# Performance work log

Measured on AMD Instinct MI355X. Metric: run time of the kernel, lower is better.

Reference implementation:

```python
import jax, jax.numpy as jnp
import numpy as np

J = 50
HEADS = 4
DIMS = [3, 64, 128, 256]
POSE_DIM = 512
B, T = 16, 128


def build_edge_index():
    # 49-bone chain over 50 joints, symmetrized, plus self-loops
    # (PyG GATConv adds self-loops by default).
    e = []
    for i in range(J - 1):
        e.append((i, i + 1))
        e.append((i + 1, i))
    for i in range(J):
        e.append((i, i))
    e = sorted(e)
    return jnp.array(e, dtype=jnp.int32).T  # [2, E]


def setup_inputs() -> dict:
    key = jax.random.key(0)
    ks = iter(jax.random.split(key, 64))
    def nrm(shape, s):
        return jax.random.normal(next(ks), shape, jnp.float32) * s
    inp = {"pose_seq": jax.random.normal(next(ks), (B, T, J, 3), jnp.float32)}
    for i in range(3):
        din, dout = DIMS[i], DIMS[i + 1]
        C = dout // HEADS
        inp[f"W{i}"] = nrm((din, dout), din ** -0.5)        # GATConv lin (no bias)
        inp[f"as{i}"] = nrm((HEADS, C), 0.1)                 # att_src
        inp[f"ad{i}"] = nrm((HEADS, C), 0.1)                 # att_dst
        inp[f"bg{i}"] = jnp.zeros((dout,), jnp.float32)      # GATConv bias
        inp[f"R{i}"] = nrm((din, dout), din ** -0.5)         # residual Linear (no bias)
        inp[f"g{i}"] = jnp.ones((dout,), jnp.float32)        # LayerNorm gamma
        inp[f"b{i}"] = jnp.zeros((dout,), jnp.float32)       # LayerNorm beta
    inp["fpW"] = nrm((J * DIMS[-1], POSE_DIM), (J * DIMS[-1]) ** -0.5)
    inp["fpb"] = jnp.zeros((POSE_DIM,), jnp.float32)
    inp["fng"] = jnp.ones((POSE_DIM,), jnp.float32)
    inp["fnb"] = jnp.zeros((POSE_DIM,), jnp.float32)
    inp["edge_index"] = build_edge_index()
    return inp


def _layer_norm(x, g, b, eps=1e-5):
    mu = jnp.mean(x, axis=-1, keepdims=True)
    var = jnp.mean(jnp.square(x - mu), axis=-1, keepdims=True)
    return (x - mu) * jax.lax.rsqrt(var + eps) * g + b


def _gat(x, src, dst, W, a_s, a_d, bias):
    # x: [G, J, Fin]; edges identical across the G graphs.
    G, Jn, _ = x.shape
    H, C = a_s.shape
    h = (x @ W).reshape(G, Jn, H, C)
    es = jnp.einsum('gjhc,hc->gjh', h, a_s)[:, src]   # [G,E,H]
    ed = jnp.einsum('gjhc,hc->gjh', h, a_d)[:, dst]
    e = jax.nn.leaky_relu(es + ed, 0.2)
    # per-destination softmax over incoming edges (per head)
    m = jnp.full((G, Jn, H), -jnp.inf, e.dtype).at[:, dst].max(e)
    m = jax.lax.stop_gradient(m)
    w = jnp.exp(e - m[:, dst])
    den = jnp.zeros((G, Jn, H), e.dtype).at[:, dst].add(w)
    alpha = w / den[:, dst]                            # [G,E,H]
    out = jnp.zeros((G, Jn, H, C), e.dtype).at[:, dst].add(alpha[..., None] * h[:, src])
    return out.reshape(G, Jn, H * C) + bias


def _forward(pose_seq, layers, fpW, fpb, fng, fnb, edge_index):
    Bb, Tt = pose_seq.shape[0], pose_seq.shape[1]
    x = pose_seq.reshape(Bb * Tt, J, 3)
    src, dst = edge_index[0], edge_index[1]
    for (W, a_s, a_d, bg, R, g, b) in layers:
        h = _gat(x, src, dst, W, a_s, a_d, bg)
        res = x @ R  # dims always change -> Linear residual (bias=False)
        x = jax.nn.gelu(_layer_norm(h + res, g, b), approximate=False)
    x = x.reshape(Bb * Tt, J * DIMS[-1]) @ fpW + fpb
    x = _layer_norm(x, fng, fnb)
    return x.reshape(Bb, Tt, POSE_DIM)


def reference(pose_seq, W0, as0, ad0, bg0, R0, g0, b0,
              W1, as1, ad1, bg1, R1, g1, b1,
              W2, as2, ad2, bg2, R2, g2, b2,
              fpW, fpb, fng, fnb, edge_index):
    layers = [(W0, as0, ad0, bg0, R0, g0, b0),
              (W1, as1, ad1, bg1, R1, g1, b1),
              (W2, as2, ad2, bg2, R2, g2, b2)]
    return _forward(pose_seq, layers, fpW, fpb, fng, fnb, edge_index)
```

## Files before the change

kernel.cpp:

```cpp
#include <hip/hip_runtime.h>
#include <hip/hip_bf16.h>
#include <math.h>

#define J 50
#define GN 2048
#define GK 12800
#define GON 512

#define SPLITK 8
#define BKC (GK / SPLITK)
#define NKT (BKC / 64)

typedef short short8 __attribute__((ext_vector_type(8)));
typedef float f32x4 __attribute__((ext_vector_type(4)));

__device__ __forceinline__ float lrelu(float x) { return x > 0.f ? x : 0.2f * x; }
__device__ __forceinline__ ushort f2bu(float f) { __hip_bfloat16 h = __float2bfloat16(f); return *(ushort*)&h; }

__device__ __forceinline__ float gelu_fast(float y) {
    float u = y * (1.f + 0.044715f * y * y);
    float t = __expf(-1.5957691216f * u);
    return y / (1.f + t);
}


template<int DIN, int KPAD, int DOUT, bool LAST>
__device__ __forceinline__ void gat_layer_v3(
    int tid, ushort* xbf, float* esW, float* Acoef, float* statsC, float* statsN,
    const ushort* __restrict__ Wt, const ushort* __restrict__ Rt,
    const ushort* __restrict__ Wex,
    const float* __restrict__ bg, const float* __restrict__ gam,
    const float* __restrict__ bet, ushort* __restrict__ gout)
{
    constexpr int NFW = DOUT / 64;
    constexpr int GRX = KPAD / 8;
    constexpr int XM  = (GRX < 8 ? GRX : 8) - 1;
    constexpr int NKS = KPAD / 32;
    const int lane = tid & 63, w = tid >> 6;
    const int lr = lane & 15, lg = lane >> 4;

    f32x4 acc[4][NFW];
    f32x4 ext[4];

    #pragma unroll
    for (int m = 0; m < 4; ++m) {
        ext[m] = (f32x4){0.f, 0.f, 0.f, 0.f};
        #pragma unroll
        for (int nf = 0; nf < NFW; ++nf) acc[m][nf] = (f32x4){0.f, 0.f, 0.f, 0.f};
    }
    #pragma unroll
    for (int ks = 0; ks < NKS; ++ks) {
        short8 af[4];
        #pragma unroll
        for (int m = 0; m < 4; ++m) {
            int row = m * 16 + lr;
            int g = (ks * 4 + lg) ^ (row & XM);
            af[m] = *(const short8*)&xbf[(row * GRX + g) * 8];
        }
        #pragma unroll
        for (int nf = 0; nf < NFW; ++nf) {
            int col = (w * NFW + nf) * 16 + lr;
            short8 bf = *(const short8*)&Wt[col * KPAD + ks * 32 + lg * 8];
            #pragma unroll
            for (int m = 0; m < 4; ++m)
                acc[m][nf] = __builtin_amdgcn_mfma_f32_16x16x32_bf16(af[m], bf, acc[m][nf], 0, 0, 0);
        }
        short8 bfe = *(const short8*)&Wex[(w * 16 + lr) * KPAD + ks * 32 + lg * 8];
        #pragma unroll
        for (int m = 0; m < 4; ++m)
            ext[m] = __builtin_amdgcn_mfma_f32_16x16x32_bf16(af[m], bfe, ext[m], 0, 0, 0);
    }

    if (lr < 2) {
        float* dstp = &esW[w * 130 + lr * 65];
        #pragma unroll
        for (int m = 0; m < 4; ++m)
            #pragma unroll
            for (int q = 0; q < 4; ++q)
                dstp[m * 16 + lg * 4 + q] = ext[m][q];
    }
    asm volatile("s_waitcnt lgkmcnt(0)" ::: "memory");

    {
        int r = lane;
        const float* ew = &esW[w * 130];
        float es0 = ew[r];
        float esm = ew[r > 0 ? r - 1 : 0];
        float esp = ew[r < 63 ? r + 1 : 63];
        float edj = ew[65 + r];
        float e1 = lrelu(es0 + edj);
        float e0 = (r > 0)     ? lrelu(esm + edj) : -1e30f;
        float e2 = (r < J - 1) ? lrelu(esp + edj) : -1e30f;
        float mx = fmaxf(e1, fmaxf(e0, e2));
        float w0 = __expf(e0 - mx), w1 = __expf(e1 - mx), w2 = __expf(e2 - mx);
        float rden = 1.f / (w0 + w1 + w2);
        Acoef[w * 192 + r]       = w0 * rden;
        Acoef[w * 192 + 64 + r]  = w1 * rden;
        Acoef[w * 192 + 128 + r] = w2 * rden;
    }
    asm volatile("s_waitcnt lgkmcnt(0)" ::: "memory");

    #pragma unroll
    for (int nf = 0; nf < NFW; ++nf) {
        float tmp[4][4];
        #pragma unroll
        for (int m = 0; m < 4; ++m) {
            int rb = m * 16 + lg * 4;
            float4 c0 = *(const float4*)&Acoef[w * 192 + rb];
            float4 c1 = *(const float4*)&Acoef[w * 192 + 64 + rb];
            float4 c2 = *(const float4*)&Acoef[w * 192 + 128 + rb];
            int mp = m > 0 ? m - 1 : 0, mn = m < 3 ? m + 1 : 3;
            float t1 = __shfl(acc[m][nf][3],  (lane + 48) & 63);
            float t2 = __shfl(acc[mp][nf][3], (lane + 48) & 63);
            float hprev = (lg > 0) ? t1 : t2;
            float b1 = __shfl(acc[m][nf][0],  (lane + 16) & 63);
            float b2 = __shfl(acc[mn][nf][0], (lane + 16) & 63);
            float hnext = (lg < 3) ? b1 : b2;
            tmp[m][0] = c0.x * hprev         + c1.x * acc[m][nf][0] + c2.x * acc[m][nf][1];
            tmp[m][1] = c0.y * acc[m][nf][0] + c1.y * acc[m][nf][1] + c2.y * acc[m][nf][2];
            tmp[m][2] = c0.z * acc[m][nf][1] + c1.z * acc[m][nf][2] + c2.z * acc[m][nf][3];
            tmp[m][3] = c0.w * acc[m][nf][2] + c1.w * acc[m][nf][3] + c2.w * hnext;
        }
        #pragma unroll
        for (int m = 0; m < 4; ++m)
            #pragma unroll
            for (int q = 0; q < 4; ++q) acc[m][nf][q] = tmp[m][q];
    }

    #pragma unroll
    for (int ks = 0; ks < NKS; ++ks) {
        short8 af[4];
        #pragma unroll
        for (int m = 0; m < 4; ++m) {
            int row = m * 16 + lr;
            int g = (ks * 4 + lg) ^ (row & XM);
            af[m] = *(const short8*)&xbf[(row * GRX + g) * 8];
        }
        #pragma unroll
        for (int nf = 0; nf < NFW; ++nf) {
            int col = (w * NFW + nf) * 16 + lr;
            short8 bf = *(const short8*)&Rt[col * KPAD + ks * 32 + lg * 8];
            #pragma unroll
            for (int m = 0; m < 4; ++m)
                acc[m][nf] = __builtin_amdgcn_mfma_f32_16x16x32_bf16(af[m], bf, acc[m][nf], 0, 0, 0);
        }
    }
    #pragma unroll
    for (int nf = 0; nf < NFW; ++nf) {
        float bgv = bg[(w * NFW + nf) * 16 + lr];
        #pragma unroll
        for (int m = 0; m < 4; ++m)
            #pragma unroll
            for (int q = 0; q < 4; ++q) acc[m][nf][q] += bgv;
    }

    #pragma unroll
    for (int m = 0; m < 4; ++m)
        #pragma unroll
        for (int q = 0; q < 4; ++q) {
            float s = 0.f, s2 = 0.f;
            #pragma unroll
            for (int nf = 0; nf < NFW; ++nf) {
                float v = acc[m][nf][q];
                s += v; s2 += v * v;
            }
            #pragma unroll
            for (int off = 1; off <= 8; off <<= 1) {
                s  += __shfl_xor(s, off, 64);
                s2 += __shfl_xor(s2, off, 64);
            }
            if (lr == 0) {
                int row = m * 16 + lg * 4 + q;
                atomicAdd(&statsC[row * 2], s);
                atomicAdd(&statsC[row * 2 + 1], s2);
            }
        }
    __syncthreads();
    if (tid < 64) {
        float S = statsC[tid * 2], S2 = statsC[tid * 2 + 1];
        float mu = S * (1.f / DOUT);
        float var = S2 * (1.f / DOUT) - mu * mu;
        statsC[tid * 2] = mu;
        statsC[tid * 2 + 1] = rsqrtf(var + 1e-5f);
    }
    __syncthreads();

    constexpr int NGR = DOUT / 8;
    constexpr int NXM = (NGR < 8 ? NGR : 8) - 1;
    #pragma unroll
    for (int nf = 0; nf < NFW; ++nf) {
        int col = (w * NFW + nf) * 16 + lr;
        float ga = gam[col], be = bet[col];
        #pragma unroll
        for (int m = 0; m < 4; ++m)
            #pragma unroll
            for (int q = 0; q < 4; ++q) {
                int row = m * 16 + lg * 4 + q;
                float mu = statsC[row * 2], inv = statsC[row * 2 + 1];
                float y = (acc[m][nf][q] - mu) * inv * ga + be;
                float ge = gelu_fast(y);
                if (LAST) {
                    if (row < J) gout[row * 256 + col] = f2bu(ge);
                } else {
                    xbf[(row * NGR + ((col >> 3) ^ (row & NXM))) * 8 + (col & 7)] =
                        (row < J) ? f2bu(ge) : (ushort)0;
                }
            }
    }
    if (tid < 128) statsN[tid] = 0.f;
    __syncthreads();
}

__global__ __launch_bounds__(256, 4) void gat_mfma(
    const float* __restrict__ pose,
    const ushort* __restrict__ Wt0, const ushort* __restrict__ Rt0,
    const ushort* __restrict__ Wt1, const ushort* __restrict__ Rt1,
    const ushort* __restrict__ Wt2, const ushort* __restrict__ Rt2,
    const ushort* __restrict__ wex0, const ushort* __restrict__ wex1,
    const ushort* __restrict__ wex2,
    const float* bg0, const float* g0v, const float* b0v,
    const float* bg1, const float* g1v, const float* b1v,
    const float* bg2, const float* g2v, const float* b2v,
    ushort* __restrict__ xg)
{
    __shared__ ushort xbf[64 * 128];
    __shared__ float esW[4 * 130];
    __shared__ float Acoef[4 * 192];
    __shared__ float sA[128], sB[128];
    int g = blockIdx.x, tid = threadIdx.x;

    for (int i = tid; i < 64 * 32; i += 256) {
        int row = i >> 5, c = i & 31;
        float v = (row < J && c < 3) ? pose[(size_t)g * (J * 3) + row * 3 + c] : 0.f;
        xbf[(row * 4 + ((c >> 3) ^ (row & 3))) * 8 + (c & 7)] = f2bu(v);
    }
    if (tid < 128) sA[tid] = 0.f;
    __syncthreads();
    gat_layer_v3<3,   32,  64, false>(tid, xbf, esW, Acoef, sA, sB, Wt0, Rt0, wex0,
                                      bg0, g0v, b0v, nullptr);
    gat_layer_v3<64,  64, 128, false>(tid, xbf, esW, Acoef, sB, sA, Wt1, Rt1, wex1,
                                      bg1, g1v, b1v, nullptr);
    gat_layer_v3<128,128, 256, true >(tid, xbf, esW, Acoef, sA, sB, Wt2, Rt2, wex2,
                                      bg2, g2v, b2v, xg + (size_t)g * GK);
}

__global__ __launch_bounds__(256) void prep_weights(
    const float* __restrict__ W0, const float* __restrict__ R0,
    const float* __restrict__ W1, const float* __restrict__ R1,
    const float* __restrict__ W2, const float* __restrict__ R2,
    ushort* __restrict__ wt)
{
    int i = blockIdx.x * 256 + threadIdx.x;
    if (i < 2048)       { int n = i >> 5, k = i & 31;                    wt[i] = f2bu(k < 3 ? W0[k * 64 + n] : 0.f); }
    else if (i < 4096)  { int j = i - 2048;  int n = j >> 5, k = j & 31; wt[i] = f2bu(k < 3 ? R0[k * 64 + n] : 0.f); }
    else if (i < 12288) { int j = i - 4096;  int n = j >> 6, k = j & 63; wt[i] = f2bu(W1[k * 128 + n]); }
    else if (i < 20480) { int j = i - 12288; int n = j >> 6, k = j & 63; wt[i] = f2bu(R1[k * 128 + n]); }
    else if (i < 53248) { int j = i - 20480; int n = j >> 7, k = j & 127; wt[i] = f2bu(W2[k * 256 + n]); }
    else if (i < 86016) { int j = i - 53248; int n = j >> 7, k = j & 127; wt[i] = f2bu(R2[k * 256 + n]); }
}

__global__ __launch_bounds__(256) void prep_wex(
    const float* __restrict__ as0, const float* __restrict__ ad0, const float* __restrict__ W0,
    const float* __restrict__ as1, const float* __restrict__ ad1, const float* __restrict__ W1,
    const float* __restrict__ as2, const float* __restrict__ ad2, const float* __restrict__ W2,
    ushort* __restrict__ wex0, ushort* __restrict__ wex1, ushort* __restrict__ wex2)
{
    int i = blockIdx.x * 256 + threadIdx.x;
    const float *as_, *ad_, *W; ushort* dst; int KPAD, DIN, DOUT, idx;
    if (i < 2048)       { idx = i;         KPAD = 32;  DIN = 3;   DOUT = 64;  as_ = as0; ad_ = ad0; W = W0; dst = wex0; }
    else if (i < 6144)  { idx = i - 2048;  KPAD = 64;  DIN = 64;  DOUT = 128; as_ = as1; ad_ = ad1; W = W1; dst = wex1; }
    else if (i < 14336) { idx = i - 6144;  KPAD = 128; DIN = 128; DOUT = 256; as_ = as2; ad_ = ad2; W = W2; dst = wex2; }
    else return;
    int k = idx % KPAD;
    int col = (idx / KPAD) & 15;
    int h = idx / (KPAD * 16);
    int C = DOUT / 4;
    float v = 0.f;
    if (col < 2 && k < DIN) {
        const float* a = (col == 0) ? as_ : ad_;
        for (int c = 0; c < C; ++c) v += W[k * DOUT + h * C + c] * a[h * C + c];
    }
    dst[idx] = f2bu(v);
}

__global__ __launch_bounds__(256) void fpw_to_bt(
    const float* __restrict__ fpW, ushort* __restrict__ Bt)
{
    __shared__ float tile[64][65];
    int kb = (blockIdx.x >> 3) * 64;
    int nb = (blockIdx.x & 7) * 64;
    int tid = threadIdx.x;
    #pragma unroll
    for (int i = 0; i < 16; ++i) {
        int idx = tid + i * 256;
        int r = idx >> 6, c = idx & 63;
        tile[r][c] = fpW[(size_t)(kb + r) * GON + nb + c];
    }
    __syncthreads();
    #pragma unroll
    for (int i = 0; i < 16; ++i) {
        int idx = tid + i * 256;
        int nr = idx >> 6, kc = idx & 63;
        Bt[(size_t)(nb + nr) * GK + kb + kc] = f2bu(tile[kc][nr]);
    }
}

__global__ __launch_bounds__(512) void final_gemm_mfma(
    const ushort* __restrict__ A,
    const ushort* __restrict__ Bt,
    float* __restrict__ parts)
{
    __shared__ ushort Asm[2][128 * 64];
    __shared__ ushort Bsm[2][128 * 64];
    int tid = threadIdx.x;
    int bid = blockIdx.x;
    int tileid = bid & 63, sp = bid >> 6;
    int rt = tileid >> 2, ct = tileid & 3;
    int ar0 = rt * 128, bc0 = ct * 128;
    int kbase = sp * BKC;

    int lane = tid & 63, wid = tid >> 6;
    int wm = wid >> 2, wn = wid & 3;

    f32x4 acc[4][2];
    #pragma unroll
    for (int mi = 0; mi < 4; ++mi)
        #pragma unroll
        for (int ni = 0; ni < 2; ++ni)
            acc[mi][ni] = (f32x4){0.f, 0.f, 0.f, 0.f};

#define STAGE(pg, k0)                                                              \
    do {                                                                           \
        _Pragma("unroll")                                                          \
        for (int s_ = 0; s_ < 4; ++s_) {                                           \
            int g_ = tid + s_ * 512;                                               \
            int gg_ = g_ & 1023;                                                   \
            int row_ = gg_ >> 3, cg_ = gg_ & 7;                                    \
            int csw_ = cg_ ^ (row_ & 7);                                           \
            const ushort* src_;                                                    \
            ushort* dst_;                                                          \
            if (g_ < 1024) {                                                       \
                src_ = A + (size_t)(ar0 + row_) * GK + (k0) + csw_ * 8;            \
                dst_ = &Asm[pg][gg_ * 8];                                          \
            } else {                                                               \
                src_ = Bt + (size_t)(bc0 + row_) * GK + (k0) + csw_ * 8;           \
                dst_ = &Bsm[pg][gg_ * 8];                                          \
            }                                                                      \
            __builtin_amdgcn_global_load_lds(                                      \
                (const __attribute__((address_space(1))) void*)src_,               \
                (__attribute__((address_space(3))) void*)dst_, 16, 0, 0);          \
        }                                                                          \
    } while (0)

    STAGE(0, kbase);
    __syncthreads();
    int pg = 0;
    for (int kt = 0; kt < NKT; ++kt) {
        if (kt + 1 < NKT) STAGE(pg ^ 1, kbase + (kt + 1) * 64);
        const ushort* Ab = Asm[pg];
        const ushort* Bb = Bsm[pg];
        short8 afr[4][2], bfr[2][2];
        #pragma unroll
        for (int mi = 0; mi < 4; ++mi)
            #pragma unroll
            for (int ks = 0; ks < 2; ++ks) {
                int row = wm * 64 + mi * 16 + (lane & 15);
                int gs = (ks * 4 + (lane >> 4)) ^ (row & 7);
                afr[mi][ks] = *(const short8*)&Ab[row * 64 + gs * 8];
            }
        #pragma unroll
        for (int ni = 0; ni < 2; ++ni)
            #pragma unroll
            for (int ks = 0; ks < 2; ++ks) {
                int row = wn * 32 + ni * 16 + (lane & 15);
                int gs = (ks * 4 + (lane >> 4)) ^ (row & 7);
                bfr[ni][ks] = *(const short8*)&Bb[row * 64 + gs * 8];
            }
        #pragma unroll
        for (int ks = 0; ks < 2; ++ks)
            #pragma unroll
            for (int mi = 0; mi < 4; ++mi)
                #pragma unroll
                for (int ni = 0; ni < 2; ++ni)
                    acc[mi][ni] = __builtin_amdgcn_mfma_f32_16x16x32_bf16(
                        afr[mi][ks], bfr[ni][ks], acc[mi][ni], 0, 0, 0);
        __syncthreads();
        pg ^= 1;
    }
#undef STAGE

    float* outp = parts + (size_t)sp * GN * GON;
    #pragma unroll
    for (int mi = 0; mi < 4; ++mi)
        #pragma unroll
        for (int ni = 0; ni < 2; ++ni)
            #pragma unroll
            for (int r = 0; r < 4; ++r) {
                int row = ar0 + wm * 64 + mi * 16 + (lane >> 4) * 4 + r;
                int col = bc0 + wn * 32 + ni * 16 + (lane & 15);
                outp[(size_t)row * GON + col] = acc[mi][ni][r];
            }
}

__global__ __launch_bounds__(256) void final_reduce_ln(
    const float* __restrict__ parts, float* __restrict__ out,
    const float* __restrict__ fpb, const float* __restrict__ fng,
    const float* __restrict__ fnb)
{
    int row = blockIdx.x * 4 + (threadIdx.x >> 6);
    int lane = threadIdx.x & 63;
    float v[8];
    float sum = 0.f;
    #pragma unroll
    for (int cc = 0; cc < 8; ++cc) {
        int o = lane + (cc << 6);
        float a = 0.f;
        #pragma unroll
        for (int s = 0; s < SPLITK; ++s)
            a += parts[(size_t)s * GN * GON + (size_t)row * GON + o];
        v[cc] = a + fpb[o];
        sum += v[cc];
    }
    #pragma unroll
    for (int off = 32; off >= 1; off >>= 1) sum += __shfl_xor(sum, off, 64);
    float mu = sum * (1.f / GON);
    float sq = 0.f;
    #pragma unroll
    for (int cc = 0; cc < 8; ++cc) { float d = v[cc] - mu; sq += d * d; }
    #pragma unroll
    for (int off = 32; off >= 1; off >>= 1) sq += __shfl_xor(sq, off, 64);
    float inv = rsqrtf(sq * (1.f / GON) + 1e-5f);
    #pragma unroll
    for (int cc = 0; cc < 8; ++cc) {
        int o = lane + (cc << 6);
        out[(size_t)row * GON + o] = (v[cc] - mu) * inv * fng[o] + fnb[o];
    }
}

extern "C" void kernel_launch(void* const* d_in, const int* in_sizes, int n_in,
                              void* d_out, int out_size, void* d_ws, size_t ws_size,
                              hipStream_t stream) {
    (void)in_sizes; (void)n_in; (void)out_size; (void)ws_size;
    const float* pose = (const float*)d_in[0];
    const float *W0 = (const float*)d_in[1],  *as0 = (const float*)d_in[2],
                *ad0 = (const float*)d_in[3], *bg0 = (const float*)d_in[4],
                *R0 = (const float*)d_in[5],  *g0v = (const float*)d_in[6],
                *b0v = (const float*)d_in[7];
    const float *W1 = (const float*)d_in[8],  *as1 = (const float*)d_in[9],
                *ad1 = (const float*)d_in[10],*bg1 = (const float*)d_in[11],
                *R1 = (const float*)d_in[12], *g1v = (const float*)d_in[13],
                *b1v = (const float*)d_in[14];
    const float *W2 = (const float*)d_in[15], *as2 = (const float*)d_in[16],
                *ad2 = (const float*)d_in[17],*bg2 = (const float*)d_in[18],
                *R2 = (const float*)d_in[19], *g2v = (const float*)d_in[20],
                *b2v = (const float*)d_in[21];
    const float* fpW = (const float*)d_in[22];
    const float* fpb = (const float*)d_in[23];
    const float* fng = (const float*)d_in[24];
    const float* fnb = (const float*)d_in[25];

    ushort* xg = (ushort*)d_ws;
    ushort* Bt = xg + (size_t)GN * GK;
    float* parts = (float*)(Bt + (size_t)GON * GK);
    ushort* wsm = (ushort*)(parts + (size_t)SPLITK * GN * GON);
    ushort *Wt0 = wsm,          *Rt0 = wsm + 2048;
    ushort *Wt1 = wsm + 4096,   *Rt1 = wsm + 12288;
    ushort *Wt2 = wsm + 20480,  *Rt2 = wsm + 53248;
    ushort* wex = wsm + 86016;
    ushort *wex0 = wex, *wex1 = wex + 2048, *wex2 = wex + 6144;
    float* out = (float*)d_out;

    prep_weights<<<336, 256, 0, stream>>>(W0, R0, W1, R1, W2, R2, wsm);
    prep_wex<<<56, 256, 0, stream>>>(as0, ad0, W0, as1, ad1, W1, as2, ad2, W2,
                                     wex0, wex1, wex2);
    fpw_to_bt<<<(GK / 64) * (GON / 64), 256, 0, stream>>>(fpW, Bt);
    gat_mfma<<<GN, 256, 0, stream>>>(pose,
        Wt0, Rt0, Wt1, Rt1, Wt2, Rt2,
        wex0, wex1, wex2,
        bg0, g0v, b0v,
        bg1, g1v, b1v,
        bg2, g2v, b2v, xg);
    final_gemm_mfma<<<64 * SPLITK, 512, 0, stream>>>(xg, Bt, parts);
    final_reduce_ln<<<GN / 4, 256, 0, stream>>>(parts, out, fpb, fng, fnb);
}
```

Measured before the change: 197.1 us.

## Process two graphs per GAT block to reuse weight fragments across twice the rows

New measurement: 523.4 us. +165.5%, slower.

```diff
diff --git a/kernel.cpp b/kernel.cpp
--- a/kernel.cpp
+++ b/kernel.cpp
@@ -25,12 +25,12 @@
 
 
 template<int DIN, int KPAD, int DOUT, bool LAST>
-__device__ __forceinline__ void gat_layer_v3(
+__device__ __forceinline__ void gat_layer_v4(
     int tid, ushort* xbf, float* esW, float* Acoef, float* statsC, float* statsN,
     const ushort* __restrict__ Wt, const ushort* __restrict__ Rt,
     const ushort* __restrict__ Wex,
     const float* __restrict__ bg, const float* __restrict__ gam,
-    const float* __restrict__ bet, ushort* __restrict__ gout)
+    const float* __restrict__ bet, ushort* __restrict__ gout0, ushort* __restrict__ gout1)
 {
     constexpr int NFW = DOUT / 64;
     constexpr int GRX = KPAD / 8;
@@ -39,20 +39,20 @@
     const int lane = tid & 63, w = tid >> 6;
     const int lr = lane & 15, lg = lane >> 4;
 
-    f32x4 acc[4][NFW];
-    f32x4 ext[4];
-
-    #pragma unroll
-    for (int m = 0; m < 4; ++m) {
+    f32x4 acc[8][NFW];
+    f32x4 ext[8];
+
+    #pragma unroll
+    for (int m = 0; m < 8; ++m) {
         ext[m] = (f32x4){0.f, 0.f, 0.f, 0.f};
         #pragma unroll
         for (int nf = 0; nf < NFW; ++nf) acc[m][nf] = (f32x4){0.f, 0.f, 0.f, 0.f};
     }
     #pragma unroll
     for (int ks = 0; ks < NKS; ++ks) {
-        short8 af[4];
-        #pragma unroll
-        for (int m = 0; m < 4; ++m) {
+        short8 af[8];
+        #pragma unroll
+        for (int m = 0; m < 8; ++m) {
             int row = m * 16 + lr;
             int g = (ks * 4 + lg) ^ (row & XM);
             af[m] = *(const short8*)&xbf[(row * GRX + g) * 8];
@@ -62,54 +62,56 @@
             int col = (w * NFW + nf) * 16 + lr;
             short8 bf = *(const short8*)&Wt[col * KPAD + ks * 32 + lg * 8];
             #pragma unroll
-            for (int m = 0; m < 4; ++m)
+            for (int m = 0; m < 8; ++m)
                 acc[m][nf] = __builtin_amdgcn_mfma_f32_16x16x32_bf16(af[m], bf, acc[m][nf], 0, 0, 0);
         }
         short8 bfe = *(const short8*)&Wex[(w * 16 + lr) * KPAD + ks * 32 + lg * 8];
         #pragma unroll
-        for (int m = 0; m < 4; ++m)
+        for (int m = 0; m < 8; ++m)
             ext[m] = __builtin_amdgcn_mfma_f32_16x16x32_bf16(af[m], bfe, ext[m], 0, 0, 0);
     }
 
     if (lr < 2) {
-        float* dstp = &esW[w * 130 + lr * 65];
-        #pragma unroll
-        for (int m = 0; m < 4; ++m)
+        float* dstp = &esW[w * 264 + lr * 132];
+        #pragma unroll
+        for (int m = 0; m < 8; ++m)
             #pragma unroll
             for (int q = 0; q < 4; ++q)
                 dstp[m * 16 + lg * 4 + q] = ext[m][q];
     }
     asm volatile("s_waitcnt lgkmcnt(0)" ::: "memory");
 
-    {
-        int r = lane;
-        const float* ew = &esW[w * 130];
+    #pragma unroll
+    for (int it = 0; it < 2; ++it) {
+        int r = lane + it * 64;
+        const float* ew = &esW[w * 264];
         float es0 = ew[r];
         float esm = ew[r > 0 ? r - 1 : 0];
-        float esp = ew[r < 63 ? r + 1 : 63];
-        float edj = ew[65 + r];
+        float esp = ew[r < 127 ? r + 1 : 127];
+        float edj = ew[132 + r];
+        int jj = r & 63;
         float e1 = lrelu(es0 + edj);
-        float e0 = (r > 0)     ? lrelu(esm + edj) : -1e30f;
-        float e2 = (r < J - 1) ? lrelu(esp + edj) : -1e30f;
+        float e0 = (jj > 0)     ? lrelu(esm + edj) : -1e30f;
+        float e2 = (jj < J - 1) ? lrelu(esp + edj) : -1e30f;
         float mx = fmaxf(e1, fmaxf(e0, e2));
         float w0 = __expf(e0 - mx), w1 = __expf(e1 - mx), w2 = __expf(e2 - mx);
         float rden = 1.f / (w0 + w1 + w2);
-        Acoef[w * 192 + r]       = w0 * rden;
-        Acoef[w * 192 + 64 + r]  = w1 * rden;
-        Acoef[w * 192 + 128 + r] = w2 * rden;
+        Acoef[w * 384 + r]       = w0 * rden;
+        Acoef[w * 384 + 128 + r] = w1 * rden;
+        Acoef[w * 384 + 256 + r] = w2 * rden;
     }
     asm volatile("s_waitcnt lgkmcnt(0)" ::: "memory");
 
     #pragma unroll
     for (int nf = 0; nf < NFW; ++nf) {
-        float tmp[4][4];
-        #pragma unroll
-        for (int m = 0; m < 4; ++m) {
+        float tmp[8][4];
+        #pragma unroll
+        for (int m = 0; m < 8; ++m) {
             int rb = m * 16 + lg * 4;
-            float4 c0 = *(const float4*)&Acoef[w * 192 + rb];
-            float4 c1 = *(const float4*)&Acoef[w * 192 + 64 + rb];
-            float4 c2 = *(const float4*)&Acoef[w * 192 + 128 + rb];
-            int mp = m > 0 ? m - 1 : 0, mn = m < 3 ? m + 1 : 3;
+            float4 c0 = *(const float4*)&Acoef[w * 384 + rb];
+            float4 c1 = *(const float4*)&Acoef[w * 384 + 128 + rb];
+            float4 c2 = *(const float4*)&Acoef[w * 384 + 256 + rb];
+            int mp = m > 0 ? m - 1 : 0, mn = m < 7 ? m + 1 : 7;
             float t1 = __shfl(acc[m][nf][3],  (lane + 48) & 63);
             float t2 = __shfl(acc[mp][nf][3], (lane + 48) & 63);
             float hprev = (lg > 0) ? t1 : t2;
@@ -122,16 +124,16 @@
             tmp[m][3] = c0.w * acc[m][nf][2] + c1.w * acc[m][nf][3] + c2.w * hnext;
         }
         #pragma unroll
-        for (int m = 0; m < 4; ++m)
+        for (int m = 0; m < 8; ++m)
             #pragma unroll
             for (int q = 0; q < 4; ++q) acc[m][nf][q] = tmp[m][q];
     }
 
     #pragma unroll
     for (int ks = 0; ks < NKS; ++ks) {
-        short8 af[4];
-        #pragma unroll
-        for (int m = 0; m < 4; ++m) {
+        short8 af[8];
+        #pragma unroll
+        for (int m = 0; m < 8; ++m) {
             int row = m * 16 + lr;
             int g = (ks * 4 + lg) ^ (row & XM);
             af[m] = *(const short8*)&xbf[(row * GRX + g) * 8];
@@ -141,7 +143,7 @@
             int col = (w * NFW + nf) * 16 + lr;
             short8 bf = *(const short8*)&Rt[col * KPAD + ks * 32 + lg * 8];
             #pragma unroll
-            for (int m = 0; m < 4; ++m)
+            for (int m = 0; m < 8; ++m)
                 acc[m][nf] = __builtin_amdgcn_mfma_f32_16x16x32_bf16(af[m], bf, acc[m][nf], 0, 0, 0);
         }
     }
@@ -149,13 +151,13 @@
     for (int nf = 0; nf < NFW; ++nf) {
         float bgv = bg[(w * NFW + nf) * 16 + lr];
         #pragma unroll
-        for (int m = 0; m < 4; ++m)
+        for (int m = 0; m < 8; ++m)
             #pragma unroll
             for (int q = 0; q < 4; ++q) acc[m][nf][q] += bgv;
     }
 
     #pragma unroll
-    for (int m = 0; m < 4; ++m)
+    for (int m = 0; m < 8; ++m)
         #pragma unroll
         for (int q = 0; q < 4; ++q) {
             float s = 0.f, s2 = 0.f;
@@ -176,7 +178,7 @@
             }
         }
     __syncthreads();
-    if (tid < 64) {
+    if (tid < 128) {
         float S = statsC[tid * 2], S2 = statsC[tid * 2 + 1];
         float mu = S * (1.f / DOUT);
         float var = S2 * (1.f / DOUT) - mu * mu;
@@ -185,33 +187,61 @@
     }
     __syncthreads();
 
-    constexpr int NGR = DOUT / 8;
-    constexpr int NXM = (NGR < 8 ? NGR : 8) - 1;
-    #pragma unroll
-    for (int nf = 0; nf < NFW; ++nf) {
-        int col = (w * NFW + nf) * 16 + lr;
-        float ga = gam[col], be = bet[col];
-        #pragma unroll
-        for (int m = 0; m < 4; ++m)
-            #pragma unroll
-            for (int q = 0; q < 4; ++q) {
-                int row = m * 16 + lg * 4 + q;
-                float mu = statsC[row * 2], inv = statsC[row * 2 + 1];
-                float y = (acc[m][nf][q] - mu) * inv * ga + be;
-                float ge = gelu_fast(y);
-                if (LAST) {
-                    if (row < J) gout[row * 256 + col] = f2bu(ge);
-                } else {
+    if (!LAST) {
+        constexpr int NGR = DOUT / 8;
+        constexpr int NXM = (NGR < 8 ? NGR : 8) - 1;
+        #pragma unroll
+        for (int nf = 0; nf < NFW; ++nf) {
+            int col = (w * NFW + nf) * 16 + lr;
+            float ga = gam[col], be = bet[col];
+            #pragma unroll
+            for (int m = 0; m < 8; ++m)
+                #pragma unroll
+                for (int q = 0; q < 4; ++q) {
+                    int row = m * 16 + lg * 4 + q;
+                    int jj = row & 63;
+                    float mu = statsC[row * 2], inv = statsC[row * 2 + 1];
+                    float y = (acc[m][nf][q] - mu) * inv * ga + be;
+                    float ge = gelu_fast(y);
                     xbf[(row * NGR + ((col >> 3) ^ (row & NXM))) * 8 + (col & 7)] =
-                        (row < J) ? f2bu(ge) : (ushort)0;
+                        (jj < J) ? f2bu(ge) : (ushort)0;
                 }
-            }
-    }
-    if (tid < 128) statsN[tid] = 0.f;
-    __syncthreads();
-}
-
-__global__ __launch_bounds__(256, 4) void gat_mfma(
+        }
+        if (tid < 256) statsN[tid] = 0.f;
+        __syncthreads();
+    } else {
+        ushort* xob = xbf;
+        #pragma unroll
+        for (int gs = 0; gs < 2; ++gs) {
+            #pragma unroll
+            for (int nf = 0; nf < NFW; ++nf) {
+                int col = (w * NFW + nf) * 16 + lr;
+                float ga = gam[col], be = bet[col];
+                #pragma unroll
+                for (int mm = 0; mm < 4; ++mm) {
+                    int m = gs * 4 + mm;
+                    #pragma unroll
+                    for (int q = 0; q < 4; ++q) {
+                        int row = m * 16 + lg * 4 + q;
+                        int jrow = row & 63;
+                        if (jrow < J) {
+                            float mu = statsC[row * 2], inv = statsC[row * 2 + 1];
+                            float y = (acc[m][nf][q] - mu) * inv * ga + be;
+                            xob[jrow * 256 + col] = f2bu(gelu_fast(y));
+                        }
+                    }
+                }
+            }
+            __syncthreads();
+            ushort* dst = gs ? gout1 : gout0;
+            for (int i = tid; i < 1600; i += 256)
+                *(short8*)(dst + i * 8) = *(const short8*)&xob[i * 8];
+            __syncthreads();
+        }
+    }
+}
+
+__global__ __launch_bounds__(256, 3) void gat_mfma(
     const float* __restrict__ pose,
     const ushort* __restrict__ Wt0, const ushort* __restrict__ Rt0,
     const ushort* __restrict__ Wt1, const ushort* __restrict__ Rt1,
@@ -223,25 +253,28 @@
     const float* bg2, const float* g2v, const float* b2v,
     ushort* __restrict__ xg)
 {
-    __shared__ ushort xbf[64 * 128];
-    __shared__ float esW[4 * 130];
-    __shared__ float Acoef[4 * 192];
-    __shared__ float sA[128], sB[128];
+    __shared__ ushort xbf[128 * 128];
+    __shared__ float esW[4 * 264];
+    __shared__ float Acoef[4 * 384];
+    __shared__ float sA[256], sB[256];
     int g = blockIdx.x, tid = threadIdx.x;
 
-    for (int i = tid; i < 64 * 32; i += 256) {
+    for (int i = tid; i < 128 * 32; i += 256) {
         int row = i >> 5, c = i & 31;
-        float v = (row < J && c < 3) ? pose[(size_t)g * (J * 3) + row * 3 + c] : 0.f;
+        int jr = row & 63, gs = row >> 6;
+        float v = (jr < J && c < 3) ? pose[((size_t)(g * 2 + gs) * J + jr) * 3 + c] : 0.f;
         xbf[(row * 4 + ((c >> 3) ^ (row & 3))) * 8 + (c & 7)] = f2bu(v);
     }
-    if (tid < 128) sA[tid] = 0.f;
+    sA[tid] = 0.f;
     __syncthreads();
-    gat_layer_v3<3,   32,  64, false>(tid, xbf, esW, Acoef, sA, sB, Wt0, Rt0, wex0,
-                                      bg0, g0v, b0v, nullptr);
-    gat_layer_v3<64,  64, 128, false>(tid, xbf, esW, Acoef, sB, sA, Wt1, Rt1, wex1,
-                                      bg1, g1v, b1v, nullptr);
-    gat_layer_v3<128,128, 256, true >(tid, xbf, esW, Acoef, sA, sB, Wt2, Rt2, wex2,
-                                      bg2, g2v, b2v, xg + (size_t)g * GK);
+    ushort* gout0 = xg + (size_t)(g * 2) * GK;
+    ushort* gout1 = xg + (size_t)(g * 2 + 1) * GK;
+    gat_layer_v4<3,   32,  64, false>(tid, xbf, esW, Acoef, sA, sB, Wt0, Rt0, wex0,
+                                      bg0, g0v, b0v, nullptr, nullptr);
+    gat_layer_v4<64,  64, 128, false>(tid, xbf, esW, Acoef, sB, sA, Wt1, Rt1, wex1,
+                                      bg1, g1v, b1v, nullptr, nullptr);
+    gat_layer_v4<128,128, 256, true >(tid, xbf, esW, Acoef, sA, sB, Wt2, Rt2, wex2,
+                                      bg2, g2v, b2v, gout0, gout1);
 }
 
 __global__ __launch_bounds__(256) void prep_weights(
@@ -474,7 +507,7 @@
     prep_wex<<<56, 256, 0, stream>>>(as0, ad0, W0, as1, ad1, W1, as2, ad2, W2,
                                      wex0, wex1, wex2);
     fpw_to_bt<<<(GK / 64) * (GON / 64), 256, 0, stream>>>(fpW, Bt);
-    gat_mfma<<<GN, 256, 0, stream>>>(pose,
+    gat_mfma<<<GN / 2, 256, 0, stream>>>(pose,
         Wt0, Rt0, Wt1, Rt1, Wt2, Rt2,
         wex0, wex1, wex2,
         bg0, g0v, b0v,
```
